# Optimization experiments

Measured on AMD Instinct MI355X. Metric: run time of the kernel, lower is better.

The kernel has to match this reference:

```python
import jax, jax.numpy as jnp
import numpy as np
import math

NUM_HEADS = 12
SPARSITY = 0.2


def setup_inputs() -> dict:
    key = jax.random.key(0)
    ks = jax.random.split(key, 4)
    B, N, C = 8, 1024, 768
    x = jax.random.normal(ks[0], (B, N, C), dtype=jnp.float32)
    origin = jax.random.normal(ks[1], (B, N, C), dtype=jnp.float32)
    W_qkv = jax.random.normal(ks[2], (C, 3 * C), dtype=jnp.float32) * (C ** -0.5)
    W_proj = jax.random.normal(ks[3], (C, C), dtype=jnp.float32) * (C ** -0.5)
    b_proj = jnp.zeros((C,), dtype=jnp.float32)
    return {"x": x, "origin": origin, "W_qkv": W_qkv, "W_proj": W_proj, "b_proj": b_proj}


def reference(x, origin, W_qkv, W_proj, b_proj):
    B, N, C = x.shape
    H = NUM_HEADS
    hd = C // H
    scale = hd ** -0.5
    # qkv projection (no bias), split into q,k,v of shape [B,H,N,hd]
    qkv = (x @ W_qkv).reshape(B, N, 3, H, hd).transpose(2, 0, 3, 1, 4)
    q, k, v = qkv[0], qkv[1], qkv[2]
    # scaled scores with constant bias log(1 + N/197); bias is constant so softmax unaffected,
    # but keep it for faithfulness (threshold is taken on post-softmax values anyway)
    logits = jnp.einsum('bhqd,bhkd->bhqk', q * scale, k) + math.log(1.0 + N / 197.0)
    attn = jax.nn.softmax(logits, axis=-1)  # [B,H,N,N]
    # global per-batch threshold: keep top sparsity fraction of all H*N*N scores
    total = H * N * N
    k_idx = int(total * SPARSITY) - 1  # index in descending order
    attn_flat = attn.reshape(B, total)
    thr = jnp.sort(attn_flat, axis=-1)[:, total - 1 - k_idx]  # ascending sort, pick k-th largest
    attn = jnp.where(attn >= thr[:, None, None, None], attn, jnp.zeros((), attn.dtype))
    # attention output, merge heads, project, residual
    out = jnp.einsum('bhqk,bhkd->bhqd', attn, v).transpose(0, 2, 1, 3).reshape(B, N, C)
    out = out @ W_proj + b_proj
    return out + origin
```

## Files before the change

kernel.cpp:

```cpp
#include <hip/hip_runtime.h>
#include <hip/hip_bf16.h>

#define BATCH 8
#define SEQ   1024
#define CDIM  768
#define HEADS 12
#define HD    64

#define NB1    2048
#define TMIN2  (-24.0f)
#define W2     (24.0f / (float)NB1)
#define INV_W2 ((float)NB1 / 24.0f)
#define HLSTR  (NB1 + 8)
#define K_SUB  629146u
#define QSCALE 0.18033688011112042f

typedef __attribute__((ext_vector_type(8)))  short bf16x8;
typedef __attribute__((ext_vector_type(4)))  short bf16x4;
typedef __attribute__((ext_vector_type(4)))  float f32x4;
typedef __attribute__((ext_vector_type(16))) float f32x16;
typedef __attribute__((ext_vector_type(4)))  unsigned u32x4;
typedef __attribute__((ext_vector_type(2)))  unsigned u32x2;

#define MFMA16(a, b, c) __builtin_amdgcn_mfma_f32_16x16x32_bf16(a, b, c, 0, 0, 0)
#define MFMA32(a, b, c) __builtin_amdgcn_mfma_f32_32x32x16_bf16(a, b, c, 0, 0, 0)
#define EXP2(x) __builtin_amdgcn_exp2f(x)
#define LOG2(x) __builtin_amdgcn_logf(x)

__device__ inline unsigned cvtpk(float lo, float hi) {
    unsigned r;
    asm("v_cvt_pk_bf16_f32 %0, %1, %2" : "=v"(r) : "v"(lo), "v"(hi));
    return r;
}

__global__ __launch_bounds__(256) void convert_x(const float* __restrict__ in,
                                                 short* __restrict__ out, int n8) {
    int i = blockIdx.x * 256 + threadIdx.x;
    if (i >= n8) return;
    float4 a = *reinterpret_cast<const float4*>(&in[(size_t)i * 8]);
    float4 b = *reinterpret_cast<const float4*>(&in[(size_t)i * 8 + 4]);
    u32x4 w = {cvtpk(a.x, a.y), cvtpk(a.z, a.w), cvtpk(b.x, b.y), cvtpk(b.z, b.w)};
    *reinterpret_cast<u32x4*>(&out[(size_t)i * 8]) = w;
}

__global__ __launch_bounds__(256) void transpose_w(const float* __restrict__ in,
                                                   short* __restrict__ out, int C) {
    __shared__ float ls[64][68];
    int r0 = blockIdx.x * 64, c0 = blockIdx.y * 64;
    int tid = threadIdx.x;
#pragma unroll
    for (int it = 0; it < 4; ++it) {
        int rr = it * 16 + (tid >> 4);
        int cc = (tid & 15) * 4;
        float4 d = *reinterpret_cast<const float4*>(&in[(size_t)(r0 + rr) * C + c0 + cc]);
        ls[rr][cc + 0] = d.x; ls[rr][cc + 1] = d.y; ls[rr][cc + 2] = d.z; ls[rr][cc + 3] = d.w;
    }
    __syncthreads();
#pragma unroll
    for (int it = 0; it < 2; ++it) {
        int orow = it * 32 + (tid >> 3);
        int oc = (tid & 7) * 8;
        u32x4 w = {cvtpk(ls[oc + 0][orow], ls[oc + 1][orow]),
                   cvtpk(ls[oc + 2][orow], ls[oc + 3][orow]),
                   cvtpk(ls[oc + 4][orow], ls[oc + 5][orow]),
                   cvtpk(ls[oc + 6][orow], ls[oc + 7][orow])};
        *reinterpret_cast<u32x4*>(&out[(size_t)(c0 + orow) * 768 + r0 + oc]) = w;
    }
}

__global__ __launch_bounds__(256) void qkv_mfma(const short* __restrict__ A,
                                                const short* __restrict__ Bt,
                                                __hip_bfloat16* __restrict__ q,
                                                __hip_bfloat16* __restrict__ k,
                                                __hip_bfloat16* __restrict__ vt) {
    const int K = 768;
    __shared__ short As[128 * 64];
    __shared__ short Bs[128 * 64];
    int tM = blockIdx.x * 128, tN = blockIdx.y * 128;
    int tid = threadIdx.x, wave = tid >> 6, lane = tid & 63, lg = lane >> 4, lc = lane & 15;
    int wr = wave >> 1, wc = wave & 1;
    int srow = tid >> 3, scol = (tid & 7) * 8;
    f32x4 acc[4][4] = {};

    bf16x8 sa[4], sb[4];
#pragma unroll
    for (int j = 0; j < 4; ++j) {
        int r = j * 32 + srow;
        sa[j] = *(const bf16x8*)&A[(size_t)(tM + r) * K + scol];
        sb[j] = *(const bf16x8*)&Bt[(size_t)(tN + r) * K + scol];
    }
#pragma unroll
    for (int j = 0; j < 4; ++j) {
        int r = j * 32 + srow;
        int sw = scol ^ ((r & 7) << 3);
        *(bf16x8*)&As[r * 64 + sw] = sa[j];
        *(bf16x8*)&Bs[r * 64 + sw] = sb[j];
    }
    __syncthreads();

    for (int kc = 0; kc < K; kc += 64) {
        if (kc + 64 < K) {
#pragma unroll
            for (int j = 0; j < 4; ++j) {
                int r = j * 32 + srow;
                sa[j] = *(const bf16x8*)&A[(size_t)(tM + r) * K + kc + 64 + scol];
                sb[j] = *(const bf16x8*)&Bt[(size_t)(tN + r) * K + kc + 64 + scol];
            }
        }
        bf16x8 af[4][2], bfr[4][2];
#pragma unroll
        for (int m4 = 0; m4 < 4; ++m4) {
            int r = wr * 64 + m4 * 16 + lc;
            int sw = (r & 7) << 3;
            af[m4][0] = *(bf16x8*)&As[r * 64 + ((lg * 8) ^ sw)];
            af[m4][1] = *(bf16x8*)&As[r * 64 + ((32 + lg * 8) ^ sw)];
        }
#pragma unroll
        for (int n4 = 0; n4 < 4; ++n4) {
            int r = wc * 64 + n4 * 16 + lc;
            int sw = (r & 7) << 3;
            bfr[n4][0] = *(bf16x8*)&Bs[r * 64 + ((lg * 8) ^ sw)];
            bfr[n4][1] = *(bf16x8*)&Bs[r * 64 + ((32 + lg * 8) ^ sw)];
        }
#pragma unroll
        for (int m4 = 0; m4 < 4; ++m4)
#pragma unroll
            for (int n4 = 0; n4 < 4; ++n4) {
                acc[m4][n4] = MFMA16(af[m4][0], bfr[n4][0], acc[m4][n4]);
                acc[m4][n4] = MFMA16(af[m4][1], bfr[n4][1], acc[m4][n4]);
            }
        __syncthreads();
        if (kc + 64 < K) {
#pragma unroll
            for (int j = 0; j < 4; ++j) {
                int r = j * 32 + srow;
                int sw = scol ^ ((r & 7) << 3);
                *(bf16x8*)&As[r * 64 + sw] = sa[j];
                *(bf16x8*)&Bs[r * 64 + sw] = sb[j];
            }
            __syncthreads();
        }
    }
    int three = tN / 768;
    int cbase = tN - three * 768 + wc * 64;
    if (three == 2) {
#pragma unroll
        for (int m4 = 0; m4 < 4; ++m4) {
            int row0 = tM + wr * 64 + m4 * 16 + lg * 4;
            int b = row0 >> 10, n0 = row0 & 1023;
#pragma unroll
            for (int n4 = 0; n4 < 4; ++n4) {
                int cw = cbase + n4 * 16 + lc;
                int h = cw >> 6, d = cw & 63;
                u32x2 w = {cvtpk(acc[m4][n4][0], acc[m4][n4][1]),
                           cvtpk(acc[m4][n4][2], acc[m4][n4][3])};
                *reinterpret_cast<u32x2*>(
                    &vt[(((size_t)(b * HEADS + h) * 64 + d) << 10) + n0]) = w;
            }
        }
    } else {
        __hip_bfloat16* dst = (three == 0) ? q : k;
#pragma unroll
        for (int m4 = 0; m4 < 4; ++m4)
#pragma unroll
            for (int n4 = 0; n4 < 4; ++n4) {
                int cw = cbase + n4 * 16 + lc;
                int h = cw >> 6, d = cw & 63;
#pragma unroll
                for (int r = 0; r < 4; r += 2) {
                    int row = tM + wr * 64 + m4 * 16 + lg * 4 + r;
                    int b = row >> 10, n = row & 1023;
                    float v0 = acc[m4][n4][r], v1 = acc[m4][n4][r + 1];
                    if (three == 0) { v0 *= QSCALE; v1 *= QSCALE; }
                    unsigned w = cvtpk(v0, v1);
                    size_t base = (((size_t)(b * HEADS + h) << 10) + n) * HD + d;
                    *(unsigned short*)&dst[base] = (unsigned short)w;
                    *(unsigned short*)&dst[base + HD] = (unsigned short)(w >> 16);
                }
            }
    }
}

__global__ __launch_bounds__(256) void stats_mfma(const short* __restrict__ q,
                                                  const short* __restrict__ k,
                                                  float* __restrict__ orow,
                                                  unsigned* __restrict__ hist) {
    __shared__ short kls[8192];
    __shared__ unsigned hl[2 * HLSTR];
    int bid = blockIdx.x;
    int grp = bid & 7;
    int bh = bid >> 3;
    int b = bh / HEADS;
    int tid = threadIdx.x, wave = tid >> 6, lane = tid & 63;
    int ql = lane & 31, h = lane >> 5;
    const short* kbase = k + (size_t)bh * SEQ * HD;
    int qrow0 = grp * 128 + wave * 32;
    const short* qbase = q + ((size_t)bh * SEQ + qrow0) * HD;
    bf16x8 qf[4];
#pragma unroll
    for (int f = 0; f < 4; ++f)
        qf[f] = *(const bf16x8*)&qbase[ql * 64 + f * 16 + h * 8];

    for (int i = tid; i < 2 * HLSTR; i += 256) hl[i] = 0;

    int srow = tid >> 3, scol = (tid & 7) * 8;

    bf16x8 st[4];
#pragma unroll
    for (int j = 0; j < 4; ++j)
        st[j] = *(const bf16x8*)&kbase[(size_t)(j * 32 + srow) * 64 + scol];
#pragma unroll
    for (int j = 0; j < 4; ++j) {
        int r = j * 32 + srow;
        *(bf16x8*)&kls[r * 64 + (scol ^ ((r & 7) << 3))] = st[j];
    }
    __syncthreads();
    float lsum = 0.f;
    for (int c = 0; c < 8; ++c) {
        if (c < 7) {
#pragma unroll
            for (int j = 0; j < 4; ++j)
                st[j] = *(const bf16x8*)&kbase[(size_t)((c + 1) * 128 + j * 32 + srow) * 64 + scol];
        }
#pragma unroll
        for (int kT = 0; kT < 4; ++kT) {
            f32x16 acc = {};
#pragma unroll
            for (int f = 0; f < 4; ++f) {
                int krow = kT * 32 + ql;
                bf16x8 af = *(bf16x8*)&kls[krow * 64 + ((f * 16 + h * 8) ^ ((krow & 7) << 3))];
                acc = MFMA32(af, qf[f], acc);
            }
            float s = 0.f;
#pragma unroll
            for (int r = 0; r < 16; ++r) s += EXP2(acc[r]);
            lsum += s;
        }
        __syncthreads();
        if (c < 7) {
#pragma unroll
            for (int j = 0; j < 4; ++j) {
                int r = j * 32 + srow;
                *(bf16x8*)&kls[r * 64 + (scol ^ ((r & 7) << 3))] = st[j];
            }
            __syncthreads();
        }
    }
    lsum += __shfl_xor(lsum, 32, 64);
    float o = LOG2(lsum);
    if (h == 0) orow[(size_t)bh * SEQ + qrow0 + ql] = o;

    f32x16 minus_o;
#pragma unroll
    for (int r = 0; r < 16; ++r) minus_o[r] = -o;

    bf16x8 sq = *(const bf16x8*)&kbase[(size_t)srow * 64 + scol];
    __syncthreads();
    *(bf16x8*)&kls[srow * 64 + (scol ^ ((srow & 7) << 3))] = sq;
    __syncthreads();
    unsigned coff = (lane & 1) * HLSTR;
    for (int c = 0; c < 8; ++c) {
        if (c < 7)
            sq = *(const bf16x8*)&kbase[(size_t)((c + 1) * 128 + srow) * 64 + scol];
        f32x16 acc = minus_o;
#pragma unroll
        for (int f = 0; f < 4; ++f) {
            bf16x8 af = *(bf16x8*)&kls[ql * 64 + ((f * 16 + h * 8) ^ ((ql & 7) << 3))];
            acc = MFMA32(af, qf[f], acc);
        }
#pragma unroll
        for (int r = 0; r < 16; ++r) {
            int bin = (int)(acc[r] * INV_W2 + (float)NB1);
            bin = bin < 0 ? 0 : (bin > NB1 - 1 ? NB1 - 1 : bin);
            atomicAdd(&hl[coff + bin], 1u);
        }
        __syncthreads();
        if (c < 7) {
            *(bf16x8*)&kls[srow * 64 + (scol ^ ((srow & 7) << 3))] = sq;
            __syncthreads();
        }
    }
    __syncthreads();
    unsigned* hb = hist + (size_t)b * NB1;
    for (int i = tid; i < NB1; i += 256) {
        unsigned s = hl[i] + hl[HLSTR + i];
        if (s) atomicAdd(&hb[i], s);
    }
}

__global__ __launch_bounds__(256) void find_thr(const unsigned* __restrict__ hist,
                                                float* __restrict__ thr) {
    __shared__ unsigned cs[256];
    int b = blockIdx.x, tid = threadIdx.x;
    const unsigned* hb = hist + (size_t)b * NB1;
    unsigned s = 0;
#pragma unroll
    for (int i = 0; i < 8; ++i) s += hb[tid * 8 + i];
    cs[tid] = s;
    __syncthreads();
    unsigned suf = 0;
    for (int j = tid; j < 256; ++j) suf += cs[j];
    unsigned above = suf - cs[tid];
    if (suf >= K_SUB && above < K_SUB) {
        unsigned acc = above;
        for (int bb = 7; bb >= 0; --bb) {
            acc += hb[tid * 8 + bb];
            if (acc >= K_SUB) {
                thr[b] = TMIN2 + (float)(tid * 8 + bb) * W2;
                break;
            }
        }
    }
}

__global__ __launch_bounds__(256) void pv_mfma(const short* __restrict__ q,
                                               const short* __restrict__ k,
                                               const short* __restrict__ vt,
                                               const float* __restrict__ orow,
                                               const float* __restrict__ thr,
                                               __hip_bfloat16* __restrict__ aout) {
    __shared__ __align__(16) char smem[32768];
    short* klsA = (short*)smem;
    short* klsB = (short*)(smem + 8192);
    short* vlsA = (short*)(smem + 16384);
    short* vlsB = (short*)(smem + 24576);
    float* comb = (float*)smem;

    int bid = blockIdx.x;
    int grp = bid & 15;
    int bh = bid >> 4;
    int b = bh / HEADS, hh = bh % HEADS;
    int tid = threadIdx.x, wave = tid >> 6, lane = tid & 63;
    int ql = lane & 31, h = lane >> 5;
    int rh = wave & 1;
    int kh = wave >> 1;
    const short* kbase = k + (size_t)bh * SEQ * HD;
    const short* vtb = vt + (size_t)bh * HD * SEQ;
    int qrow0 = grp * 64 + rh * 32;
    const short* qbase = q + ((size_t)bh * SEQ + qrow0) * HD;
    bf16x8 qf[4];
#pragma unroll
    for (int f = 0; f < 4; ++f)
        qf[f] = *(const bf16x8*)&qbase[ql * 64 + f * 16 + h * 8];
    float o = orow[(size_t)bh * SEQ + qrow0 + ql];
    float tt = thr[b];
    f32x16 oacc[2] = {};
    f32x16 minus_o;
#pragma unroll
    for (int r = 0; r < 16; ++r) minus_o[r] = -o;

    short* kls = kh ? klsB : klsA;
    short* vls = kh ? vlsB : vlsA;

    int sp = tid >> 7;
    int tl = tid & 127;
    int srow = tl >> 3, scol = (tl & 7) * 8;
    short* skls = sp ? klsB : klsA;
    short* svls = sp ? vlsB : vlsA;

    bf16x8 sk[4], sv[4];
    int cc0 = sp * 8;
#pragma unroll
    for (int j = 0; j < 4; ++j) {
        int r = j * 16 + srow;
        sk[j] = *(const bf16x8*)&kbase[(size_t)(cc0 * 64 + r) * 64 + scol];
        sv[j] = *(const bf16x8*)&vtb[((size_t)r << 10) + cc0 * 64 + scol];
    }
#pragma unroll
    for (int j = 0; j < 4; ++j) {
        int r = j * 16 + srow;
        *(bf16x8*)&skls[r * 64 + (scol ^ ((r & 7) << 3))] = sk[j];
        *(bf16x8*)&svls[r * 64 + (scol ^ ((r & 7) << 3))] = sv[j];
    }
    __syncthreads();

    for (int c = 0; c < 8; ++c) {
        if (c < 7) {
            int cc = sp * 8 + c + 1;
#pragma unroll
            for (int j = 0; j < 4; ++j) {
                int r = j * 16 + srow;
                sk[j] = *(const bf16x8*)&kbase[(size_t)(cc * 64 + r) * 64 + scol];
                sv[j] = *(const bf16x8*)&vtb[((size_t)r << 10) + cc * 64 + scol];
            }
        }
#pragma unroll
        for (int kT = 0; kT < 2; ++kT) {
            f32x16 acc = minus_o;
#pragma unroll
            for (int f = 0; f < 4; ++f) {
                int krow = kT * 32 + ql;
                bf16x8 af = *(bf16x8*)&kls[krow * 64 + ((f * 16 + h * 8) ^ ((krow & 7) << 3))];
                acc = MFMA32(af, qf[f], acc);
            }
            float p[16];
#pragma unroll
            for (int r = 0; r < 16; ++r)
                p[r] = (acc[r] >= tt) ? EXP2(acc[r]) : 0.f;
            unsigned c8[8];
#pragma unroll
            for (int i = 0; i < 8; ++i) c8[i] = cvtpk(p[2 * i], p[2 * i + 1]);
#pragma unroll
            for (int s = 0; s < 2; ++s) {
                unsigned a1 = c8[4 * s],     b1 = c8[4 * s + 2];
                unsigned a2 = c8[4 * s + 1], b2 = c8[4 * s + 3];
                asm("v_permlane32_swap_b32 %0, %1" : "+v"(a1), "+v"(b1));
                asm("v_permlane32_swap_b32 %0, %1" : "+v"(a2), "+v"(b2));
                u32x4 W = {a1, a2, b1, b2};
                bf16x8 pa = __builtin_bit_cast(bf16x8, W);
#pragma unroll
                for (int dt = 0; dt < 2; ++dt) {
                    int vrow = dt * 32 + ql;
                    int vcol = (kT * 32 + s * 16 + h * 8) ^ ((vrow & 7) << 3);
                    bf16x8 vf = *(bf16x8*)&vls[vrow * 64 + vcol];
                    oacc[dt] = MFMA32(pa, vf, oacc[dt]);
                }
            }
        }
        __syncthreads();
        if (c < 7) {
#pragma unroll
            for (int j = 0; j < 4; ++j) {
                int r = j * 16 + srow;
                *(bf16x8*)&skls[r * 64 + (scol ^ ((r & 7) << 3))] = sk[j];
                *(bf16x8*)&svls[r * 64 + (scol ^ ((r & 7) << 3))] = sv[j];
            }
            __syncthreads();
        }
    }

    if (kh == 1) {
#pragma unroll
        for (int dt = 0; dt < 2; ++dt)
#pragma unroll
            for (int r = 0; r < 16; ++r) {
                int crow = (r & 3) + 8 * (r >> 2) + 4 * h;
                comb[(rh * 32 + crow) * 65 + dt * 32 + ql] = oacc[dt][r];
            }
    }
    __syncthreads();
    if (kh == 1) return;
#pragma unroll
    for (int dt = 0; dt < 2; ++dt)
#pragma unroll
        for (int r = 0; r < 16; ++r) {
            int crow = (r & 3) + 8 * (r >> 2) + 4 * h;
            oacc[dt][r] += comb[(rh * 32 + crow) * 65 + dt * 32 + ql];
        }
#pragma unroll
    for (int dt = 0; dt < 2; ++dt)
#pragma unroll
        for (int r = 0; r < 16; r += 2) {
            int qr0 = qrow0 + (r & 3) + 8 * (r >> 2) + 4 * h;
            int qr1 = qrow0 + ((r + 1) & 3) + 8 * ((r + 1) >> 2) + 4 * h;
            unsigned w = cvtpk(oacc[dt][r], oacc[dt][r + 1]);
            *(unsigned short*)&aout[((size_t)b * SEQ + qr0) * CDIM + hh * 64 + dt * 32 + ql] =
                (unsigned short)w;
            *(unsigned short*)&aout[((size_t)b * SEQ + qr1) * CDIM + hh * 64 + dt * 32 + ql] =
                (unsigned short)(w >> 16);
        }
}

__global__ __launch_bounds__(256) void proj_mfma(const short* __restrict__ A,
                                                 const short* __restrict__ Bt,
                                                 const float* __restrict__ bias,
                                                 const float* __restrict__ origin,
                                                 float* __restrict__ out) {
    const int K = 768, NN = 768;
    __shared__ short As[128 * 64];
    __shared__ short Bs[128 * 64];
    int tM = blockIdx.x * 128, tN = blockIdx.y * 128;
    int tid = threadIdx.x, wave = tid >> 6, lane = tid & 63, lg = lane >> 4, lc = lane & 15;
    int wr = wave >> 1, wc = wave & 1;
    int srow = tid >> 3, scol = (tid & 7) * 8;
    f32x4 acc[4][4] = {};

    bf16x8 sa[4], sb[4];
#pragma unroll
    for (int j = 0; j < 4; ++j) {
        int r = j * 32 + srow;
        sa[j] = *(const bf16x8*)&A[(size_t)(tM + r) * K + scol];
        sb[j] = *(const bf16x8*)&Bt[(size_t)(tN + r) * K + scol];
    }
#pragma unroll
    for (int j = 0; j < 4; ++j) {
        int r = j * 32 + srow;
        int sw = scol ^ ((r & 7) << 3);
        *(bf16x8*)&As[r * 64 + sw] = sa[j];
        *(bf16x8*)&Bs[r * 64 + sw] = sb[j];
    }
    __syncthreads();

    for (int kc = 0; kc < K; kc += 64) {
        if (kc + 64 < K) {
#pragma unroll
            for (int j = 0; j < 4; ++j) {
                int r = j * 32 + srow;
                sa[j] = *(const bf16x8*)&A[(size_t)(tM + r) * K + kc + 64 + scol];
                sb[j] = *(const bf16x8*)&Bt[(size_t)(tN + r) * K + kc + 64 + scol];
            }
        }
        bf16x8 af[4][2], bfr[4][2];
#pragma unroll
        for (int m4 = 0; m4 < 4; ++m4) {
            int r = wr * 64 + m4 * 16 + lc;
            int sw = (r & 7) << 3;
            af[m4][0] = *(bf16x8*)&As[r * 64 + ((lg * 8) ^ sw)];
            af[m4][1] = *(bf16x8*)&As[r * 64 + ((32 + lg * 8) ^ sw)];
        }
#pragma unroll
        for (int n4 = 0; n4 < 4; ++n4) {
            int r = wc * 64 + n4 * 16 + lc;
            int sw = (r & 7) << 3;
            bfr[n4][0] = *(bf16x8*)&Bs[r * 64 + ((lg * 8) ^ sw)];
            bfr[n4][1] = *(bf16x8*)&Bs[r * 64 + ((32 + lg * 8) ^ sw)];
        }
#pragma unroll
        for (int m4 = 0; m4 < 4; ++m4)
#pragma unroll
            for (int n4 = 0; n4 < 4; ++n4) {
                acc[m4][n4] = MFMA16(af[m4][0], bfr[n4][0], acc[m4][n4]);
                acc[m4][n4] = MFMA16(af[m4][1], bfr[n4][1], acc[m4][n4]);
            }
        __syncthreads();
        if (kc + 64 < K) {
#pragma unroll
            for (int j = 0; j < 4; ++j) {
                int r = j * 32 + srow;
                int sw = scol ^ ((r & 7) << 3);
                *(bf16x8*)&As[r * 64 + sw] = sa[j];
                *(bf16x8*)&Bs[r * 64 + sw] = sb[j];
            }
            __syncthreads();
        }
    }
#pragma unroll
    for (int m4 = 0; m4 < 4; ++m4)
#pragma unroll
        for (int n4 = 0; n4 < 4; ++n4)
#pragma unroll
            for (int r = 0; r < 4; ++r) {
                int row = tM + wr * 64 + m4 * 16 + lg * 4 + r;
                int col = tN + wc * 64 + n4 * 16 + lc;
                out[(size_t)row * NN + col] = acc[m4][n4][r] + bias[col] + origin[(size_t)row * NN + col];
            }
}

extern "C" void kernel_launch(void* const* d_in, const int* in_sizes, int n_in,
                              void* d_out, int out_size, void* d_ws, size_t ws_size,
                              hipStream_t stream) {
    const float* x      = (const float*)d_in[0];
    const float* origin = (const float*)d_in[1];
    const float* W_qkv  = (const float*)d_in[2];
    const float* W_proj = (const float*)d_in[3];
    const float* b_proj = (const float*)d_in[4];
    float* out = (float*)d_out;
    char* ws = (char*)d_ws;

    const size_t QKV_ELEMS = (size_t)BATCH * HEADS * SEQ * HD;
    const size_t X_ELEMS   = (size_t)BATCH * SEQ * CDIM;
    size_t off = 0;
    short* xb  = (short*)(ws + off); off += X_ELEMS * 2;
    short* wqt = (short*)(ws + off); off += (size_t)2304 * 768 * 2;
    short* wpt = (short*)(ws + off); off += (size_t)768 * 768 * 2;
    short* q   = (short*)(ws + off); off += QKV_ELEMS * 2;
    short* k   = (short*)(ws + off); off += QKV_ELEMS * 2;
    short* vt  = (short*)(ws + off); off += QKV_ELEMS * 2;
    short* aoutb = (short*)(ws + off); off += QKV_ELEMS * 2;
    float* orow = (float*)(ws + off); off += (size_t)BATCH * HEADS * SEQ * 4;
    unsigned* hist = (unsigned*)(ws + off); off += (size_t)BATCH * NB1 * 4;
    float* thr = (float*)(ws + off); off += 8 * 4;

    hipMemsetAsync(hist, 0, (size_t)BATCH * NB1 * sizeof(unsigned), stream);
    convert_x<<<dim3((X_ELEMS / 8 + 255) / 256), 256, 0, stream>>>(x, xb, (int)(X_ELEMS / 8));
    transpose_w<<<dim3(12, 36), 256, 0, stream>>>(W_qkv, wqt, 2304);
    transpose_w<<<dim3(12, 12), 256, 0, stream>>>(W_proj, wpt, 768);
    qkv_mfma<<<dim3(64, 18), 256, 0, stream>>>(xb, wqt,
                                               (__hip_bfloat16*)q, (__hip_bfloat16*)k, (__hip_bfloat16*)vt);
    stats_mfma<<<dim3(BATCH * HEADS * 8), 256, 0, stream>>>(q, k, orow, hist);
    find_thr<<<dim3(BATCH), 256, 0, stream>>>(hist, thr);
    pv_mfma<<<dim3(BATCH * HEADS * 16), 256, 0, stream>>>(q, k, vt, orow, thr,
                                                          (__hip_bfloat16*)aoutb);
    proj_mfma<<<dim3(64, 6), 256, 0, stream>>>(aoutb, wpt, b_proj, origin, out);
}
```

Before: 171.8 us.

## Fuse prep kernels and build histogram from cached subsampled scores

Merges the x conversion and both weight transposes into one launch to cut launch overhead. In the stats kernel, the histogram pass no longer recomputes QK^T over a second sweep of K. Instead it caches bf16-packed logits from the first key tile of every other chunk during the sum pass and bins those. The subsample constant K_SUB is halved to match. This removes a full MFMA pass plus its LDS reloads and barriers, but the threshold estimate now uses half as many samples at bf16 precision, which could shift the chosen threshold.

```diff
diff --git a/kernel.cpp b/kernel.cpp
--- a/kernel.cpp
+++ b/kernel.cpp
@@ -12,7 +12,7 @@
 #define W2     (24.0f / (float)NB1)
 #define INV_W2 ((float)NB1 / 24.0f)
 #define HLSTR  (NB1 + 8)
-#define K_SUB  629146u
+#define K_SUB  314573u
 #define QSCALE 0.18033688011112042f
 
 typedef __attribute__((ext_vector_type(8)))  short bf16x8;
@@ -33,21 +33,28 @@
     return r;
 }
 
-__global__ __launch_bounds__(256) void convert_x(const float* __restrict__ in,
-                                                 short* __restrict__ out, int n8) {
-    int i = blockIdx.x * 256 + threadIdx.x;
-    if (i >= n8) return;
-    float4 a = *reinterpret_cast<const float4*>(&in[(size_t)i * 8]);
-    float4 b = *reinterpret_cast<const float4*>(&in[(size_t)i * 8 + 4]);
-    u32x4 w = {cvtpk(a.x, a.y), cvtpk(a.z, a.w), cvtpk(b.x, b.y), cvtpk(b.z, b.w)};
-    *reinterpret_cast<u32x4*>(&out[(size_t)i * 8]) = w;
-}
-
-__global__ __launch_bounds__(256) void transpose_w(const float* __restrict__ in,
-                                                   short* __restrict__ out, int C) {
+__global__ __launch_bounds__(256) void prep_all(const float* __restrict__ x,
+                                                const float* __restrict__ Wq,
+                                                const float* __restrict__ Wp,
+                                                short* __restrict__ xb,
+                                                short* __restrict__ wqt,
+                                                short* __restrict__ wpt) {
     __shared__ float ls[64][68];
-    int r0 = blockIdx.x * 64, c0 = blockIdx.y * 64;
-    int tid = threadIdx.x;
+    int bid = blockIdx.x, tid = threadIdx.x;
+    if (bid < 3072) {
+        int i = bid * 256 + tid;
+        float4 a = *reinterpret_cast<const float4*>(&x[(size_t)i * 8]);
+        float4 b = *reinterpret_cast<const float4*>(&x[(size_t)i * 8 + 4]);
+        u32x4 w = {cvtpk(a.x, a.y), cvtpk(a.z, a.w), cvtpk(b.x, b.y), cvtpk(b.z, b.w)};
+        *reinterpret_cast<u32x4*>(&xb[(size_t)i * 8]) = w;
+        return;
+    }
+    const float* in;
+    short* out;
+    int C, t;
+    if (bid < 3504) { t = bid - 3072; in = Wq; out = wqt; C = 2304; }
+    else            { t = bid - 3504; in = Wp; out = wpt; C = 768; }
+    int r0 = (t % 12) * 64, c0 = (t / 12) * 64;
 #pragma unroll
     for (int it = 0; it < 4; ++it) {
         int rr = it * 16 + (tid >> 4);
@@ -204,6 +211,7 @@
     for (int i = tid; i < 2 * HLSTR; i += 256) hl[i] = 0;
 
     int srow = tid >> 3, scol = (tid & 7) * 8;
+    unsigned scache[4][8];
 
     bf16x8 st[4];
 #pragma unroll
@@ -216,6 +224,7 @@
     }
     __syncthreads();
     float lsum = 0.f;
+#pragma unroll
     for (int c = 0; c < 8; ++c) {
         if (c < 7) {
 #pragma unroll
@@ -231,6 +240,11 @@
                 bf16x8 af = *(bf16x8*)&kls[krow * 64 + ((f * 16 + h * 8) ^ ((krow & 7) << 3))];
                 acc = MFMA32(af, qf[f], acc);
             }
+            if (kT == 0 && (c & 1) == 0) {
+#pragma unroll
+                for (int i = 0; i < 8; ++i)
+                    scache[c >> 1][i] = cvtpk(acc[2 * i], acc[2 * i + 1]);
+            }
             float s = 0.f;
 #pragma unroll
             for (int r = 0; r < 16; ++r) s += EXP2(acc[r]);
@@ -250,36 +264,21 @@
     float o = LOG2(lsum);
     if (h == 0) orow[(size_t)bh * SEQ + qrow0 + ql] = o;
 
-    f32x16 minus_o;
-#pragma unroll
-    for (int r = 0; r < 16; ++r) minus_o[r] = -o;
-
-    bf16x8 sq = *(const bf16x8*)&kbase[(size_t)srow * 64 + scol];
-    __syncthreads();
-    *(bf16x8*)&kls[srow * 64 + (scol ^ ((srow & 7) << 3))] = sq;
-    __syncthreads();
     unsigned coff = (lane & 1) * HLSTR;
-    for (int c = 0; c < 8; ++c) {
-        if (c < 7)
-            sq = *(const bf16x8*)&kbase[(size_t)((c + 1) * 128 + srow) * 64 + scol];
-        f32x16 acc = minus_o;
-#pragma unroll
-        for (int f = 0; f < 4; ++f) {
-            bf16x8 af = *(bf16x8*)&kls[ql * 64 + ((f * 16 + h * 8) ^ ((ql & 7) << 3))];
-            acc = MFMA32(af, qf[f], acc);
-        }
-#pragma unroll
-        for (int r = 0; r < 16; ++r) {
-            int bin = (int)(acc[r] * INV_W2 + (float)NB1);
-            bin = bin < 0 ? 0 : (bin > NB1 - 1 ? NB1 - 1 : bin);
-            atomicAdd(&hl[coff + bin], 1u);
-        }
-        __syncthreads();
-        if (c < 7) {
-            *(bf16x8*)&kls[srow * 64 + (scol ^ ((srow & 7) << 3))] = sq;
-            __syncthreads();
-        }
-    }
+#pragma unroll
+    for (int cc = 0; cc < 4; ++cc)
+#pragma unroll
+        for (int i = 0; i < 8; ++i) {
+            unsigned w = scache[cc][i];
+            float s0 = __builtin_bit_cast(float, w << 16);
+            float s1 = __builtin_bit_cast(float, w & 0xffff0000u);
+            int b0 = (int)((s0 - o) * INV_W2 + (float)NB1);
+            int b1 = (int)((s1 - o) * INV_W2 + (float)NB1);
+            b0 = b0 < 0 ? 0 : (b0 > NB1 - 1 ? NB1 - 1 : b0);
+            b1 = b1 < 0 ? 0 : (b1 > NB1 - 1 ? NB1 - 1 : b1);
+            atomicAdd(&hl[coff + b0], 1u);
+            atomicAdd(&hl[coff + b1], 1u);
+        }
     __syncthreads();
     unsigned* hb = hist + (size_t)b * NB1;
     for (int i = tid; i < NB1; i += 256) {
@@ -572,9 +571,7 @@
     float* thr = (float*)(ws + off); off += 8 * 4;
 
     hipMemsetAsync(hist, 0, (size_t)BATCH * NB1 * sizeof(unsigned), stream);
-    convert_x<<<dim3((X_ELEMS / 8 + 255) / 256), 256, 0, stream>>>(x, xb, (int)(X_ELEMS / 8));
-    transpose_w<<<dim3(12, 36), 256, 0, stream>>>(W_qkv, wqt, 2304);
-    transpose_w<<<dim3(12, 12), 256, 0, stream>>>(W_proj, wpt, 768);
+    prep_all<<<dim3(3648), 256, 0, stream>>>(x, W_qkv, W_proj, xb, wqt, wpt);
     qkv_mfma<<<dim3(64, 18), 256, 0, stream>>>(xb, wqt,
                                                (__hip_bfloat16*)q, (__hip_bfloat16*)k, (__hip_bfloat16*)vt);
     stats_mfma<<<dim3(BATCH * HEADS * 8), 256, 0, stream>>>(q, k, orow, hist);
```

Result: faster. 164.7 us (-4.2%).
